# Kernel optimization log

Measured on AMD Instinct MI355X. Metric: run time of the kernel, lower is better.

Reference implementation:

```python
import jax, jax.numpy as jnp
import numpy as np
from jax import lax

MARGIN = 1.0
LAMDA = 0.003
EPS = 1e-9


def extract_features(f, idx):
    # f: (B,C,h,w); idx: (B,N,2) int with idx[...,0]=x, idx[...,1]=y -> (B*N, C)
    B, N = idx.shape[:2]
    b = jnp.arange(B)[:, None]
    x = idx[..., 0]
    y = idx[..., 1]
    g = f[b, :, y, x]  # (B, N, C)
    return g.reshape(B * N, f.shape[1])


def grad_axis(f, axis):
    # np.gradient along one axis: central differences, one-sided at edges
    fl = jnp.moveaxis(f, axis, 0)
    g = jnp.concatenate([
        fl[1:2] - fl[0:1],
        (fl[2:] - fl[:-2]) * 0.5,
        fl[-1:] - fl[-2:-1],
    ], axis=0)
    return jnp.moveaxis(g, 0, axis)


def contrastive(fa, fb, N, pos):
    diff = fa - fb
    if pos:
        return jnp.sum(diff * diff / N)
    m = jnp.maximum(MARGIN - diff, 0.0)
    return jnp.sum(m * m / N)


def gn_loss(f_t, fb, ub):
    # f_t: (B*N, C) target features; fb: (B,C,h,w); ub: (B,N,2) int matches
    B, N = ub.shape[:2]
    xs = ub  # deterministic stand-in for round(rand + ub) rejection sampling
    f_s = extract_features(fb, xs)
    r = f_s - f_t  # (BN, C)
    fbd = lax.stop_gradient(fb)  # original uses fb.detach() for gradients
    gy = grad_axis(fbd, 2)
    gx = grad_axis(fbd, 3)
    Jx = extract_features(gx, xs)  # (BN, C)
    Jy = extract_features(gy, xs)
    J = jnp.stack([Jx, Jy], axis=-1)  # (BN, C, 2)
    H = jnp.einsum('nci,ncj->nij', J, J) + EPS * jnp.eye(2, dtype=fb.dtype)
    b = jnp.einsum('nci,nc->ni', J, r)  # (BN, 2)
    xsf = xs.reshape(B * N, 2).astype(fb.dtype)
    miu = xsf - jnp.einsum('nij,nj->ni', jnp.linalg.inv(H), b)
    d = ub.reshape(B * N, 2).astype(fb.dtype) - miu
    e1 = 0.5 * jnp.sum(jnp.einsum('na,nab,nb->n', d, H, d))
    log_det = jnp.log(jnp.linalg.det(H))
    e2 = B * N * jnp.log(jnp.asarray(2.0 * np.pi, fb.dtype)) - 0.5 * jnp.sum(log_det)
    return e1 + e2


def gn_forward(F_a, F_b, ka, kb, na, nb):
    N = ka.shape[1]
    fa4 = extract_features(F_a[-1], ka)
    fb4 = extract_features(F_b[-1], kb)
    loss = 0.0
    for i in range(4):
        level = 2 ** (3 - i)
        if i == 3:
            fa_pos, fb_pos = fa4, fb4
        else:
            fa_pos = extract_features(F_a[i], ka // level)
            fb_pos = extract_features(F_b[i], kb // level)
        fa_neg = extract_features(F_a[i], na // level)
        fb_neg = extract_features(F_b[i], nb // level)
        loss_pos = contrastive(fa_pos, fb_pos, N, pos=True)
        loss_neg = contrastive(fa_neg, fb_neg, N, pos=False)
        loss_gn = gn_loss(fa_pos, F_b[i], kb // level)
        loss = loss_pos + loss_neg + LAMDA * loss_gn + loss
    return loss


def setup_inputs() -> dict:
    key = jax.random.key(0)
    ks = jax.random.split(key, 12)
    B, C, H, W, N = 4, 64, 256, 256, 512
    inp = {}
    for j, (name, s) in enumerate([
        ('fa0', 32), ('fa1', 64), ('fa2', 128), ('fa3', 256),
        ('fb0', 32), ('fb1', 64), ('fb2', 128), ('fb3', 256)]):
        inp[name] = jax.random.normal(ks[j], (B, C, s, s), dtype=jnp.float32)
    for j, name in enumerate(['ka', 'kb', 'na', 'nb']):
        inp[name] = jax.random.randint(ks[8 + j], (B, N, 2), 0, 256, dtype=jnp.int32)
    return inp


def reference(fa0, fa1, fa2, fa3, fb0, fb1, fb2, fb3, ka, kb, na, nb):
    F_a = [fa0, fa1, fa2, fa3]
    F_b = [fb0, fb1, fb2, fb3]
    return gn_forward(F_a, F_b, ka, kb, na, nb)
```

## Files before the change

### kernel.cpp

```cpp
#include <hip/hip_runtime.h>

#define MARGIN 1.0f
#define LAMDA  0.003f
#define EPS_H  1e-9f

#define E2_CONST (0.003f * 4.0f * 2048.0f * 1.8378770664093453f)

__device__ __forceinline__ float finalize_level(const float* v) {
    const float Hxx = v[2] + EPS_H;
    const float Hxy = v[3];
    const float Hyy = v[4] + EPS_H;
    const float bX  = v[5];
    const float bY  = v[6];
    const float det = Hxx * Hyy - Hxy * Hxy;
    const float e1  = 0.5f * (Hyy * bX * bX - 2.0f * Hxy * bX * bY + Hxx * bY * bY) / det;
    return (v[0] + v[1]) * (1.0f / 512.0f) + LAMDA * (e1 - 0.5f * logf(det));
}

__device__ __forceinline__ void gather7(
    const float* __restrict__ fa, const float* __restrict__ fb,
    int2 kA, int2 kB, int2 nA, int2 nB,
    int shift, int S, int plane, float* v)
{
    const int kax = kA.x >> shift, kay = kA.y >> shift;
    const int kbx = kB.x >> shift, kby = kB.y >> shift;
    const int nax = nA.x >> shift, nay = nA.y >> shift;
    const int nbx = nB.x >> shift, nby = nB.y >> shift;

    const float va  = fa[plane + kay * S + kax];
    const float vna = fa[plane + nay * S + nax];
    const float vb  = fb[plane + kby * S + kbx];
    const float vnb = fb[plane + nby * S + nbx];

    const int   xm = (kbx > 0)     ? kbx - 1 : 0;
    const int   xp = (kbx < S - 1) ? kbx + 1 : S - 1;
    const float sx = (kbx > 0 && kbx < S - 1) ? 0.5f : 1.0f;
    const int   ym = (kby > 0)     ? kby - 1 : 0;
    const int   yp = (kby < S - 1) ? kby + 1 : S - 1;
    const float sy = (kby > 0 && kby < S - 1) ? 0.5f : 1.0f;
    const float Jx = (fb[plane + kby * S + xp] - fb[plane + kby * S + xm]) * sx;
    const float Jy = (fb[plane + yp * S + kbx] - fb[plane + ym * S + kbx]) * sy;

    const float dpos = va - vb;
    const float dneg = vna - vnb;
    const float mneg = fmaxf(MARGIN - dneg, 0.0f);
    const float r    = vb - va;

    v[0] = dpos * dpos;
    v[1] = mneg * mneg;
    v[2] = Jx * Jx;
    v[3] = Jx * Jy;
    v[4] = Jy * Jy;
    v[5] = Jx * r;
    v[6] = Jy * r;
}

__global__ __launch_bounds__(256) void gn_task_kernel(
    const float* __restrict__ fa0, const float* __restrict__ fa1,
    const float* __restrict__ fa2, const float* __restrict__ fa3,
    const float* __restrict__ fb0, const float* __restrict__ fb1,
    const float* __restrict__ fb2, const float* __restrict__ fb3,
    const int* __restrict__ ka, const int* __restrict__ kb,
    const int* __restrict__ na, const int* __restrict__ nb,
    float* __restrict__ out)
{
    __shared__ float l3sums[2][7];
    __shared__ float wloss[2];

    const int wave = threadIdx.x >> 6;
    const int lane = threadIdx.x & 63;
    const int n    = blockIdx.x;
    const int b    = n >> 9;

    const int2 kA = ((const int2*)ka)[n];
    const int2 kB = ((const int2*)kb)[n];
    const int2 nA = ((const int2*)na)[n];
    const int2 nB = ((const int2*)nb)[n];

    if (wave < 2) {
        const int role = lane >> 5;
        const int c    = (wave << 5) + (lane & 31);
        const int plane = (b * 64 + c) * (256 * 256);

        const int a0v = plane + kA.y * 256 + kA.x;
        const int a1v = plane + nA.y * 256 + nA.x;
        const int a2v = plane + kB.y * 256 + kB.x;
        const int a3v = plane + nB.y * 256 + nB.x;

        const int kbx = kB.x, kby = kB.y;
        const int xm = (kbx > 0)   ? kbx - 1 : 0;
        const int xp = (kbx < 255) ? kbx + 1 : 255;
        const float sx = (kbx > 0 && kbx < 255) ? 0.5f : 1.0f;
        const int ym = (kby > 0)   ? kby - 1 : 0;
        const int yp = (kby < 255) ? kby + 1 : 255;
        const float sy = (kby > 0 && kby < 255) ? 0.5f : 1.0f;
        const int a0g = plane + kby * 256 + xm;
        const int a1g = plane + kby * 256 + xp;
        const int a2g = plane + ym * 256 + kbx;
        const int a3g = plane + yp * 256 + kbx;

        const float* p0 = role ? fb3 : fa3;
        const float* p1 = role ? fb3 : fa3;
        const int a0 = role ? a0g : a0v;
        const int a1 = role ? a1g : a1v;
        const int a2 = role ? a2g : a2v;
        const int a3 = role ? a3g : a3v;

        const float L0 = p0[a0];
        const float L1 = p1[a1];
        const float L2 = fb3[a2];
        const float L3 = fb3[a3];

        const float r    = L2 - L0;
        const float rsw  = __shfl_xor(r, 32, 64);
        const float Jx   = (L1 - L0) * sx;
        const float Jy   = (L3 - L2) * sy;
        const float dpos = L0 - L2;
        const float dneg = L1 - L3;
        const float mneg = fmaxf(MARGIN - dneg, 0.0f);

        float v[7];
        v[0] = role ? 0.0f : dpos * dpos;
        v[1] = role ? 0.0f : mneg * mneg;
        v[2] = role ? Jx * Jx  : 0.0f;
        v[3] = role ? Jx * Jy  : 0.0f;
        v[4] = role ? Jy * Jy  : 0.0f;
        v[5] = role ? Jx * rsw : 0.0f;
        v[6] = role ? Jy * rsw : 0.0f;

        #pragma unroll
        for (int mask = 32; mask >= 1; mask >>= 1)
            #pragma unroll
            for (int t = 0; t < 7; ++t)
                v[t] += __shfl_xor(v[t], mask, 64);

        if (lane == 0)
            #pragma unroll
            for (int t = 0; t < 7; ++t) l3sums[wave][t] = v[t];
    } else if (wave == 2) {
        float v[7];
        const int plane = (b * 64 + lane) * (128 * 128);
        gather7(fa2, fb2, kA, kB, nA, nB, 1, 128, plane, v);
        #pragma unroll
        for (int mask = 32; mask >= 1; mask >>= 1)
            #pragma unroll
            for (int t = 0; t < 7; ++t)
                v[t] += __shfl_xor(v[t], mask, 64);
        if (lane == 0) wloss[0] = finalize_level(v);
    } else {
        float v[14];
        const int plane1 = (b * 64 + lane) * (64 * 64);
        const int plane0 = (b * 64 + lane) * (32 * 32);
        gather7(fa1, fb1, kA, kB, nA, nB, 2, 64, plane1, v);
        gather7(fa0, fb0, kA, kB, nA, nB, 3, 32, plane0, v + 7);
        #pragma unroll
        for (int mask = 32; mask >= 1; mask >>= 1)
            #pragma unroll
            for (int t = 0; t < 14; ++t)
                v[t] += __shfl_xor(v[t], mask, 64);
        if (lane == 0) wloss[1] = finalize_level(v) + finalize_level(v + 7);
    }

    __syncthreads();
    if (threadIdx.x == 0) {
        float v3[7];
        #pragma unroll
        for (int t = 0; t < 7; ++t) v3[t] = l3sums[0][t] + l3sums[1][t];
        float s = finalize_level(v3) + wloss[0] + wloss[1];
        if (blockIdx.x == 0) s += E2_CONST;
        atomicAdd(out, s);
    }
}

extern "C" void kernel_launch(void* const* d_in, const int* in_sizes, int n_in,
                              void* d_out, int out_size, void* d_ws, size_t ws_size,
                              hipStream_t stream) {
    const float* fa0 = (const float*)d_in[0];
    const float* fa1 = (const float*)d_in[1];
    const float* fa2 = (const float*)d_in[2];
    const float* fa3 = (const float*)d_in[3];
    const float* fb0 = (const float*)d_in[4];
    const float* fb1 = (const float*)d_in[5];
    const float* fb2 = (const float*)d_in[6];
    const float* fb3 = (const float*)d_in[7];
    const int*   ka  = (const int*)d_in[8];
    const int*   kb  = (const int*)d_in[9];
    const int*   na  = (const int*)d_in[10];
    const int*   nb  = (const int*)d_in[11];

    float* out = (float*)d_out;
    hipMemsetAsync(out, 0, sizeof(float), stream);

    gn_task_kernel<<<2048, 256, 0, stream>>>(fa0, fa1, fa2, fa3,
                                             fb0, fb1, fb2, fb3,
                                             ka, kb, na, nb, out);
}
```

Measured before the change: 55.57 us.

## Assign one wave per pyramid level and use nontemporal loads for level 3

```diff
diff --git a/kernel.cpp b/kernel.cpp
--- a/kernel.cpp
+++ b/kernel.cpp
@@ -5,6 +5,12 @@
 #define EPS_H  1e-9f
 
 #define E2_CONST (0.003f * 4.0f * 2048.0f * 1.8378770664093453f)
+
+template <bool NT>
+__device__ __forceinline__ float ldf(const float* __restrict__ p) {
+    if (NT) return __builtin_nontemporal_load(p);
+    return *p;
+}
 
 __device__ __forceinline__ float finalize_level(const float* v) {
     const float Hxx = v[2] + EPS_H;
@@ -17,6 +23,7 @@
     return (v[0] + v[1]) * (1.0f / 512.0f) + LAMDA * (e1 - 0.5f * logf(det));
 }
 
+template <bool NT>
 __device__ __forceinline__ void gather7(
     const float* __restrict__ fa, const float* __restrict__ fb,
     int2 kA, int2 kB, int2 nA, int2 nB,
@@ -27,19 +34,24 @@
     const int nax = nA.x >> shift, nay = nA.y >> shift;
     const int nbx = nB.x >> shift, nby = nB.y >> shift;
 
-    const float va  = fa[plane + kay * S + kax];
-    const float vna = fa[plane + nay * S + nax];
-    const float vb  = fb[plane + kby * S + kbx];
-    const float vnb = fb[plane + nby * S + nbx];
-
     const int   xm = (kbx > 0)     ? kbx - 1 : 0;
     const int   xp = (kbx < S - 1) ? kbx + 1 : S - 1;
     const float sx = (kbx > 0 && kbx < S - 1) ? 0.5f : 1.0f;
     const int   ym = (kby > 0)     ? kby - 1 : 0;
     const int   yp = (kby < S - 1) ? kby + 1 : S - 1;
     const float sy = (kby > 0 && kby < S - 1) ? 0.5f : 1.0f;
-    const float Jx = (fb[plane + kby * S + xp] - fb[plane + kby * S + xm]) * sx;
-    const float Jy = (fb[plane + yp * S + kbx] - fb[plane + ym * S + kbx]) * sy;
+
+    const float va  = ldf<NT>(fa + plane + kay * S + kax);
+    const float vna = ldf<NT>(fa + plane + nay * S + nax);
+    const float vb  = ldf<NT>(fb + plane + kby * S + kbx);
+    const float vnb = ldf<NT>(fb + plane + nby * S + nbx);
+    const float gxm = ldf<NT>(fb + plane + kby * S + xm);
+    const float gxp = ldf<NT>(fb + plane + kby * S + xp);
+    const float gym = ldf<NT>(fb + plane + ym * S + kbx);
+    const float gyp = ldf<NT>(fb + plane + yp * S + kbx);
+
+    const float Jx = (gxp - gxm) * sx;
+    const float Jy = (gyp - gym) * sy;
 
     const float dpos = va - vb;
     const float dneg = vna - vnb;
@@ -64,109 +76,46 @@
     const int* __restrict__ na, const int* __restrict__ nb,
     float* __restrict__ out)
 {
-    __shared__ float l3sums[2][7];
-    __shared__ float wloss[2];
+    __shared__ float wloss[4];
 
-    const int wave = threadIdx.x >> 6;
-    const int lane = threadIdx.x & 63;
-    const int n    = blockIdx.x;
-    const int b    = n >> 9;
+    const int wave  = threadIdx.x >> 6;
+    const int lane  = threadIdx.x & 63;
+    const int level = wave;
+    const int n     = blockIdx.x;
+    const int b     = n >> 9;
+    const int shift = 3 - level;
+    const int S     = 32 << level;
 
     const int2 kA = ((const int2*)ka)[n];
     const int2 kB = ((const int2*)kb)[n];
     const int2 nA = ((const int2*)na)[n];
     const int2 nB = ((const int2*)nb)[n];
 
-    if (wave < 2) {
-        const int role = lane >> 5;
-        const int c    = (wave << 5) + (lane & 31);
-        const int plane = (b * 64 + c) * (256 * 256);
+    const int plane = (b * 64 + lane) * (S * S);
 
-        const int a0v = plane + kA.y * 256 + kA.x;
-        const int a1v = plane + nA.y * 256 + nA.x;
-        const int a2v = plane + kB.y * 256 + kB.x;
-        const int a3v = plane + nB.y * 256 + nB.x;
+    float v[7];
+    if (level == 3) {
+        gather7<true>(fa3, fb3, kA, kB, nA, nB, 0, 256, plane, v);
+    } else if (level == 2) {
+        gather7<false>(fa2, fb2, kA, kB, nA, nB, 1, 128, plane, v);
+    } else if (level == 1) {
+        gather7<false>(fa1, fb1, kA, kB, nA, nB, 2, 64, plane, v);
+    } else {
+        gather7<false>(fa0, fb0, kA, kB, nA, nB, 3, 32, plane, v);
+    }
 
-        const int kbx = kB.x, kby = kB.y;
-        const int xm = (kbx > 0)   ? kbx - 1 : 0;
-        const int xp = (kbx < 255) ? kbx + 1 : 255;
-        const float sx = (kbx > 0 && kbx < 255) ? 0.5f : 1.0f;
-        const int ym = (kby > 0)   ? kby - 1 : 0;
-        const int yp = (kby < 255) ? kby + 1 : 255;
-        const float sy = (kby > 0 && kby < 255) ? 0.5f : 1.0f;
-        const int a0g = plane + kby * 256 + xm;
-        const int a1g = plane + kby * 256 + xp;
-        const int a2g = plane + ym * 256 + kbx;
-        const int a3g = plane + yp * 256 + kbx;
+    #pragma unroll
+    for (int mask = 32; mask >= 1; mask >>= 1)
+        #pragma unroll
+        for (int t = 0; t < 7; ++t)
+            v[t] += __shfl_xor(v[t], mask, 64);
 
-        const float* p0 = role ? fb3 : fa3;
-        const float* p1 = role ? fb3 : fa3;
-        const int a0 = role ? a0g : a0v;
-        const int a1 = role ? a1g : a1v;
-        const int a2 = role ? a2g : a2v;
-        const int a3 = role ? a3g : a3v;
-
-        const float L0 = p0[a0];
-        const float L1 = p1[a1];
-        const float L2 = fb3[a2];
-        const float L3 = fb3[a3];
-
-        const float r    = L2 - L0;
-        const float rsw  = __shfl_xor(r, 32, 64);
-        const float Jx   = (L1 - L0) * sx;
-        const float Jy   = (L3 - L2) * sy;
-        const float dpos = L0 - L2;
-        const float dneg = L1 - L3;
-        const float mneg = fmaxf(MARGIN - dneg, 0.0f);
-
-        float v[7];
-        v[0] = role ? 0.0f : dpos * dpos;
-        v[1] = role ? 0.0f : mneg * mneg;
-        v[2] = role ? Jx * Jx  : 0.0f;
-        v[3] = role ? Jx * Jy  : 0.0f;
-        v[4] = role ? Jy * Jy  : 0.0f;
-        v[5] = role ? Jx * rsw : 0.0f;
-        v[6] = role ? Jy * rsw : 0.0f;
-
-        #pragma unroll
-        for (int mask = 32; mask >= 1; mask >>= 1)
-            #pragma unroll
-            for (int t = 0; t < 7; ++t)
-                v[t] += __shfl_xor(v[t], mask, 64);
-
-        if (lane == 0)
-            #pragma unroll
-            for (int t = 0; t < 7; ++t) l3sums[wave][t] = v[t];
-    } else if (wave == 2) {
-        float v[7];
-        const int plane = (b * 64 + lane) * (128 * 128);
-        gather7(fa2, fb2, kA, kB, nA, nB, 1, 128, plane, v);
-        #pragma unroll
-        for (int mask = 32; mask >= 1; mask >>= 1)
-            #pragma unroll
-            for (int t = 0; t < 7; ++t)
-                v[t] += __shfl_xor(v[t], mask, 64);
-        if (lane == 0) wloss[0] = finalize_level(v);
-    } else {
-        float v[14];
-        const int plane1 = (b * 64 + lane) * (64 * 64);
-        const int plane0 = (b * 64 + lane) * (32 * 32);
-        gather7(fa1, fb1, kA, kB, nA, nB, 2, 64, plane1, v);
-        gather7(fa0, fb0, kA, kB, nA, nB, 3, 32, plane0, v + 7);
-        #pragma unroll
-        for (int mask = 32; mask >= 1; mask >>= 1)
-            #pragma unroll
-            for (int t = 0; t < 14; ++t)
-                v[t] += __shfl_xor(v[t], mask, 64);
-        if (lane == 0) wloss[1] = finalize_level(v) + finalize_level(v + 7);
-    }
+    if (lane == 0)
+        wloss[wave] = finalize_level(v);
 
     __syncthreads();
     if (threadIdx.x == 0) {
-        float v3[7];
-        #pragma unroll
-        for (int t = 0; t < 7; ++t) v3[t] = l3sums[0][t] + l3sums[1][t];
-        float s = finalize_level(v3) + wloss[0] + wloss[1];
+        float s = wloss[0] + wloss[1] + wloss[2] + wloss[3];
         if (blockIdx.x == 0) s += E2_CONST;
         atomicAdd(out, s);
     }
```

After: 52.61 us. -5.3%, faster.
